# Kernel optimization log

Measured on AMD Instinct MI355X. Metric: run time of the kernel, lower is better.

The kernel has to match this reference:

```python
import jax, jax.numpy as jnp
import numpy as np


def setup_inputs() -> dict:
    key = jax.random.key(0)
    k1, k2 = jax.random.split(key)
    support_features = jax.random.normal(k1, (1000, 5, 512), dtype=jnp.float32)
    query_features = jax.random.normal(k2, (5000, 512), dtype=jnp.float32)
    return {"support_features": support_features, "query_features": query_features, "use_cosine": 1}


def reference(support_features, query_features, use_cosine):
    # Preprocess: mean-center over (classes, shots), then L2-normalize per vector.
    mean = jnp.mean(support_features, axis=(0, 1), keepdims=True)  # [1,1,D]
    s = support_features - mean                                    # [C,S,D]
    q = query_features - mean[0]                                   # [Q,D]
    s = s / jnp.linalg.norm(s, axis=2, keepdims=True)
    q = q / jnp.linalg.norm(q, axis=1, keepdims=True)
    if use_cosine:
        # cosine sims without materializing [C,Q,S,D]; einsum fuses the dot.
        sims = jnp.einsum('csd,qd->cqs', s, q)   # [C,Q,S]
        best = jnp.max(sims, axis=2)             # [C,Q] best shot per class
        return jnp.argmax(best, axis=0)          # [Q] predicted class
    else:
        # euclidean cdist(query[Q,D], support[C,S,D]) -> [C,Q,S]
        d2 = (jnp.sum(q * q, axis=1)[None, :, None]
              + jnp.sum(s * s, axis=2)[:, None, :]
              - 2.0 * jnp.einsum('csd,qd->cqs', s, q))
        dist = jnp.sqrt(jnp.maximum(d2, 0.0))
        best = jnp.min(dist, axis=2)
        return jnp.argmin(best, axis=0)
```

## Files before the change

### kernel.cpp

```cpp
#include <hip/hip_runtime.h>
#include <stdint.h>

#define D     512
#define NSUP  5000
#define NQRY  5000
#define NPAD  5120
#define MEAN_BLOCKS 100
#define ROWS_PER_MEAN_BLOCK 50
#define SCALE 512.0f

#define OFF_SHI     0
#define OFF_SLO     5242880
#define OFF_QHI     10485760
#define OFF_QLO     15728640
#define OFF_PARTIAL 20971520
#define OFF_MEAN    21176320
#define OFF_KEYS    21178368

#define SH_SHI   0
#define SH_SLO   32768
#define SH_QHI   65536
#define SH_QLO   98304
#define SH_KL    131072
#define SH_TOTAL (131072 + 2048)

typedef _Float16 half4v __attribute__((ext_vector_type(4)));
typedef _Float16 half8v __attribute__((ext_vector_type(8)));
typedef float    f32x4  __attribute__((ext_vector_type(4)));

__device__ __forceinline__ unsigned long long pack_key(float v, int sidx) {
    unsigned u = __float_as_uint(v);
    u = (u & 0x80000000u) ? ~u : (u | 0x80000000u);
    return ((unsigned long long)u << 32) | (unsigned)(0xFFFFFFFFu - (unsigned)sidx);
}

__device__ __forceinline__ void gload16(const void* g, void* l) {
    __builtin_amdgcn_global_load_lds(
        (const __attribute__((address_space(1))) unsigned int*)g,
        (__attribute__((address_space(3))) unsigned int*)l, 16, 0, 0);
}

__global__ void k_partial_mean(const float* __restrict__ sup, float* __restrict__ partial) {
    const int col = threadIdx.x;
    const int b   = blockIdx.x;
    const int r0  = b * ROWS_PER_MEAN_BLOCK;
    float acc = 0.0f;
    #pragma unroll 5
    for (int r = 0; r < ROWS_PER_MEAN_BLOCK; ++r)
        acc += sup[(size_t)(r0 + r) * D + col];
    partial[b * D + col] = acc;
}

__global__ void k_mean_init(const float* __restrict__ partial, float* __restrict__ mean,
                            unsigned long long* __restrict__ keys) {
    const int col = threadIdx.x;
    float acc = 0.0f;
    #pragma unroll 4
    for (int b = 0; b < MEAN_BLOCKS; ++b) acc += partial[b * D + col];
    mean[col] = acc * (1.0f / (float)NSUP);
    for (int i = col; i < NSUP; i += 512) keys[i] = 0ull;
}

__global__ void k_split(const float* __restrict__ sup, const float* __restrict__ qry,
                        const float* __restrict__ mean,
                        _Float16* __restrict__ shi, _Float16* __restrict__ slo,
                        _Float16* __restrict__ qhi, _Float16* __restrict__ qlo) {
    const int t    = threadIdx.x;
    const int rloc = t >> 7;
    const int tc   = t & 127;
    const int b    = (int)blockIdx.x * 4 + rloc;
    const float* src; _Float16 *dhi, *dlo; int valid;
    if (b < NPAD) { src = sup + (size_t)b * D;
                    dhi = shi + (size_t)b * D; dlo = slo + (size_t)b * D; valid = (b < NSUP); }
    else          { int r = b - NPAD; src = qry + (size_t)r * D;
                    dhi = qhi + (size_t)r * D; dlo = qlo + (size_t)r * D; valid = (r < NQRY); }
    __shared__ float red[8];
    if (!valid) {
        half4v z = {};
        *(half4v*)(dhi + tc * 4) = z;
        *(half4v*)(dlo + tc * 4) = z;
        return;
    }
    float4 v = *(const float4*)(src + tc * 4);
    float4 m = *(const float4*)(mean + tc * 4);
    v.x -= m.x; v.y -= m.y; v.z -= m.z; v.w -= m.w;
    float ss = v.x * v.x + v.y * v.y + v.z * v.z + v.w * v.w;
    #pragma unroll
    for (int off = 32; off > 0; off >>= 1) ss += __shfl_down(ss, off, 64);
    if ((t & 63) == 0) red[t >> 6] = ss;
    __syncthreads();
    const float rn = SCALE / sqrtf(red[rloc * 2] + red[rloc * 2 + 1]);
    float sv[4] = {v.x * rn, v.y * rn, v.z * rn, v.w * rn};
    half4v h, l;
    #pragma unroll
    for (int i = 0; i < 4; ++i) {
        _Float16 hh = (_Float16)sv[i];
        h[i] = hh;
        l[i] = (_Float16)(sv[i] - (float)hh);
    }
    *(half4v*)(dhi + tc * 4) = h;
    *(half4v*)(dlo + tc * 4) = l;
}

__launch_bounds__(512, 2)
__global__ void k_main(const _Float16* __restrict__ shi, const _Float16* __restrict__ slo,
                       const _Float16* __restrict__ qhi, const _Float16* __restrict__ qlo,
                       unsigned long long* __restrict__ keys) {
    extern __shared__ char smem[];
    char* lshi = smem + SH_SHI;
    char* lslo = smem + SH_SLO;
    char* lqhi = smem + SH_QHI;
    char* lqlo = smem + SH_QLO;
    unsigned long long* kl = (unsigned long long*)(smem + SH_KL);

    const int tid  = threadIdx.x;
    const int lane = tid & 63;
    const int wv   = tid >> 6;
    const int q0   = blockIdx.x * 256;
    const int s0   = blockIdx.y * 256;
    const int wr   = wv >> 2;
    const int wc   = wv & 3;

    if (tid < 256) kl[tid] = 0ull;

    const int srow = wv * 16 + (lane >> 2);
    const int sl0  = ((lane & 3) ^ ((lane >> 3) & 3)) * 16;
    const size_t gA0 = (size_t)(s0 + srow) * 1024 + sl0;
    const size_t gB0 = (size_t)(q0 + srow) * 1024 + sl0;
    const char* pShi = (const char*)shi; const char* pSlo = (const char*)slo;
    const char* pQhi = (const char*)qhi; const char* pQlo = (const char*)qlo;
    const int dst0 = wv * 1024;
    const int dst1 = 8192 + wv * 1024;

    const int l15 = lane & 15;
    const int kg  = lane >> 4;
    const int swz = (kg ^ ((l15 >> 1) & 3)) * 16;
    const int foA = (wr * 128 + l15) * 64 + swz;
    const int foB = (wc * 64  + l15) * 64 + swz;

    f32x4 acc[8][4] = {};

#define BAR()    asm volatile("s_barrier" ::: "memory")
#define WAITV6() asm volatile("s_waitcnt vmcnt(6)" ::: "memory")
#define WAITV4() asm volatile("s_waitcnt vmcnt(4)" ::: "memory")

#define ST2(P, KT, K2) do { const size_t kb_ = (size_t)(KT) * 64;           \
        if ((K2) == 0) {                                                    \
            gload16(pShi + gA0 + kb_,          lshi + (P) * 16384 + dst0);  \
            gload16(pShi + gA0 + 131072 + kb_, lshi + (P) * 16384 + dst1);  \
        } else if ((K2) == 1) {                                             \
            gload16(pSlo + gA0 + kb_,          lslo + (P) * 16384 + dst0);  \
            gload16(pSlo + gA0 + 131072 + kb_, lslo + (P) * 16384 + dst1);  \
        } else if ((K2) == 2) {                                             \
            gload16(pQhi + gB0 + kb_,          lqhi + (P) * 16384 + dst0);  \
            gload16(pQhi + gB0 + 131072 + kb_, lqhi + (P) * 16384 + dst1);  \
        } else {                                                            \
            gload16(pQlo + gB0 + kb_,          lqlo + (P) * 16384 + dst0);  \
            gload16(pQlo + gB0 + 131072 + kb_, lqlo + (P) * 16384 + dst1);  \
        } } while (0)

#define MMA32(AV, BV) do {                                                  \
        __builtin_amdgcn_s_setprio(1);                                      \
        _Pragma("unroll")                                                   \
        for (int fa_ = 0; fa_ < 8; ++fa_)                                   \
        { _Pragma("unroll")                                                 \
          for (int fb_ = 0; fb_ < 4; ++fb_) {                               \
            acc[fa_][fb_] = __builtin_amdgcn_mfma_f32_16x16x32_f16(         \
                AV[fa_], BV[fb_], acc[fa_][fb_], 0, 0, 0);                  \
          } }                                                               \
        __builtin_amdgcn_s_setprio(0);                                      \
        __builtin_amdgcn_sched_barrier(0);                                  \
    } while (0)

    ST2(0, 0, 0); ST2(0, 0, 2); ST2(0, 0, 1); ST2(0, 0, 3);
    WAITV4();
    BAR();

    for (int t = 0; t < 16; ++t) {
        const int P  = t & 1;
        const int Pn = P ^ 1;
        const int tn = (t + 1) & 15;
        half8v ah[8], al[8], bh[4], bl[4];

        #pragma unroll
        for (int f = 0; f < 8; ++f)
            ah[f] = *(const half8v*)(lshi + P * 16384 + foA + f * 1024);
        #pragma unroll
        for (int j = 0; j < 4; ++j)
            bh[j] = *(const half8v*)(lqhi + P * 16384 + foB + j * 1024);
        ST2(Pn, tn, 0);
        ST2(Pn, tn, 2);
        MMA32(ah, bh);
        WAITV6();
        BAR();

        #pragma unroll
        for (int f = 0; f < 8; ++f)
            al[f] = *(const half8v*)(lslo + P * 16384 + foA + f * 1024);
        ST2(Pn, tn, 1);
        MMA32(al, bh);
        WAITV6();
        BAR();

        #pragma unroll
        for (int j = 0; j < 4; ++j)
            bl[j] = *(const half8v*)(lqlo + P * 16384 + foB + j * 1024);
        ST2(Pn, tn, 3);
        MMA32(ah, bl);
        WAITV4();
        BAR();
    }

#undef MMA32
#undef ST2

    #pragma unroll
    for (int fb = 0; fb < 4; ++fb) {
        unsigned long long best = 0ull;
        #pragma unroll
        for (int fa = 0; fa < 8; ++fa)
            #pragma unroll
            for (int r = 0; r < 4; ++r) {
                const int s = s0 + wr * 128 + fa * 16 + kg * 4 + r;
                if (s < NSUP) {
                    unsigned long long k = pack_key(acc[fa][fb][r], s);
                    if (k > best) best = k;
                }
            }
        unsigned long long o = __shfl_xor(best, 16, 64); if (o > best) best = o;
        o = __shfl_xor(best, 32, 64);                    if (o > best) best = o;
        if (kg == 0) atomicMax(&kl[wc * 64 + fb * 16 + l15], best);
    }
    __syncthreads();
    if (tid < 256) {
        const int q = q0 + tid;
        if (q < NQRY && kl[tid] != 0ull) atomicMax(&keys[q], kl[tid]);
    }
#undef BAR
#undef WAITV6
#undef WAITV4
}

__global__ void k_decode(const unsigned long long* __restrict__ keys, int* __restrict__ out) {
    const int q = blockIdx.x * 256 + threadIdx.x;
    if (q < NQRY) {
        unsigned sidx = 0xFFFFFFFFu - (unsigned)(keys[q] & 0xFFFFFFFFull);
        out[q] = (int)(sidx / 5u);
    }
}

extern "C" void kernel_launch(void* const* d_in, const int* in_sizes, int n_in,
                              void* d_out, int out_size, void* d_ws, size_t ws_size,
                              hipStream_t stream) {
    const float* sup = (const float*)d_in[0];
    const float* qry = (const float*)d_in[1];
    int* out = (int*)d_out;

    char* ws = (char*)d_ws;
    _Float16* shi = (_Float16*)(ws + OFF_SHI);
    _Float16* slo = (_Float16*)(ws + OFF_SLO);
    _Float16* qhi = (_Float16*)(ws + OFF_QHI);
    _Float16* qlo = (_Float16*)(ws + OFF_QLO);
    float* partial = (float*)(ws + OFF_PARTIAL);
    float* mean    = (float*)(ws + OFF_MEAN);
    unsigned long long* keys = (unsigned long long*)(ws + OFF_KEYS);

    static bool attr_set = false;
    if (!attr_set) {
        (void)hipFuncSetAttribute((const void*)k_main,
                                  hipFuncAttributeMaxDynamicSharedMemorySize, SH_TOTAL);
        attr_set = true;
    }

    k_partial_mean<<<MEAN_BLOCKS, 512, 0, stream>>>(sup, partial);
    k_mean_init<<<1, 512, 0, stream>>>(partial, mean, keys);
    k_split<<<(2 * NPAD) / 4, 512, 0, stream>>>(sup, qry, mean, shi, slo, qhi, qlo);
    dim3 grid(NPAD / 256, NPAD / 256);
    k_main<<<grid, 512, SH_TOTAL, stream>>>(shi, slo, qhi, qlo, keys);
    k_decode<<<(NQRY + 255) / 256, 256, 0, stream>>>(keys, out);
}
```

Baseline: 163.9 us.

## Fuse mean reduction and decode into neighbours using last-block atomic counters

Merges the partial-mean and mean-finalize kernels into one kernel in which the last block to finish, found through an atomic counter, computes the mean. It also folds the decode step into the tail of the main GEMM kernel with a second last-block counter, and peels the final k-iteration so no wasted prefetch is issued. The aim is to cut two kernel launches and the idle gaps between them, at the cost of an added memset, extra fences, and a serial decode done by a single block.

```diff
diff --git a/kernel.cpp b/kernel.cpp
--- a/kernel.cpp
+++ b/kernel.cpp
@@ -5,8 +5,6 @@
 #define NSUP  5000
 #define NQRY  5000
 #define NPAD  5120
-#define MEAN_BLOCKS 100
-#define ROWS_PER_MEAN_BLOCK 50
 #define SCALE 512.0f
 
 #define OFF_SHI     0
@@ -16,13 +14,15 @@
 #define OFF_PARTIAL 20971520
 #define OFF_MEAN    21176320
 #define OFF_KEYS    21178368
+#define OFF_CTR     21218368
 
 #define SH_SHI   0
 #define SH_SLO   32768
 #define SH_QHI   65536
 #define SH_QLO   98304
 #define SH_KL    131072
-#define SH_TOTAL (131072 + 2048)
+#define SH_DM    133120
+#define SH_TOTAL 133136
 
 typedef _Float16 half4v __attribute__((ext_vector_type(4)));
 typedef _Float16 half8v __attribute__((ext_vector_type(8)));
@@ -40,25 +40,31 @@
         (__attribute__((address_space(3))) unsigned int*)l, 16, 0, 0);
 }
 
-__global__ void k_partial_mean(const float* __restrict__ sup, float* __restrict__ partial) {
+__global__ void k_prep(const float* __restrict__ sup, float* __restrict__ partial,
+                       float* __restrict__ mean, unsigned long long* __restrict__ keys,
+                       unsigned int* __restrict__ ctr) {
     const int col = threadIdx.x;
     const int b   = blockIdx.x;
-    const int r0  = b * ROWS_PER_MEAN_BLOCK;
     float acc = 0.0f;
     #pragma unroll 5
-    for (int r = 0; r < ROWS_PER_MEAN_BLOCK; ++r)
-        acc += sup[(size_t)(r0 + r) * D + col];
+    for (int r = 0; r < 50; ++r)
+        acc += sup[(size_t)(b * 50 + r) * D + col];
     partial[b * D + col] = acc;
-}
-
-__global__ void k_mean_init(const float* __restrict__ partial, float* __restrict__ mean,
-                            unsigned long long* __restrict__ keys) {
-    const int col = threadIdx.x;
-    float acc = 0.0f;
-    #pragma unroll 4
-    for (int b = 0; b < MEAN_BLOCKS; ++b) acc += partial[b * D + col];
-    mean[col] = acc * (1.0f / (float)NSUP);
-    for (int i = col; i < NSUP; i += 512) keys[i] = 0ull;
+    if (col < 50) keys[b * 50 + col] = 0ull;
+    __threadfence();
+    __syncthreads();
+    __shared__ unsigned int done;
+    if (col == 0)
+        done = __hip_atomic_fetch_add(ctr, 1u, __ATOMIC_ACQ_REL, __HIP_MEMORY_SCOPE_AGENT);
+    __syncthreads();
+    if (done == 99) {
+        float m = 0.0f;
+        #pragma unroll 4
+        for (int bb = 0; bb < 100; ++bb)
+            m += __hip_atomic_load(&partial[bb * D + col],
+                                   __ATOMIC_RELAXED, __HIP_MEMORY_SCOPE_AGENT);
+        mean[col] = m * (1.0f / (float)NSUP);
+    }
 }
 
 __global__ void k_split(const float* __restrict__ sup, const float* __restrict__ qry,
@@ -105,7 +111,8 @@
 __launch_bounds__(512, 2)
 __global__ void k_main(const _Float16* __restrict__ shi, const _Float16* __restrict__ slo,
                        const _Float16* __restrict__ qhi, const _Float16* __restrict__ qlo,
-                       unsigned long long* __restrict__ keys) {
+                       unsigned long long* __restrict__ keys, int* __restrict__ out,
+                       unsigned int* __restrict__ ctr) {
     extern __shared__ char smem[];
     char* lshi = smem + SH_SHI;
     char* lslo = smem + SH_SLO;
@@ -143,6 +150,8 @@
 #define BAR()    asm volatile("s_barrier" ::: "memory")
 #define WAITV6() asm volatile("s_waitcnt vmcnt(6)" ::: "memory")
 #define WAITV4() asm volatile("s_waitcnt vmcnt(4)" ::: "memory")
+#define WAITV2() asm volatile("s_waitcnt vmcnt(2)" ::: "memory")
+#define WAITV0() asm volatile("s_waitcnt vmcnt(0)" ::: "memory")
 
 #define ST2(P, KT, K2) do { const size_t kb_ = (size_t)(KT) * 64;           \
         if ((K2) == 0) {                                                    \
@@ -159,6 +168,15 @@
             gload16(pQlo + gB0 + 131072 + kb_, lqlo + (P) * 16384 + dst1);  \
         } } while (0)
 
+#define RD_AH(P) do { _Pragma("unroll") for (int f = 0; f < 8; ++f)         \
+        ah[f] = *(const half8v*)(lshi + (P) * 16384 + foA + f * 1024); } while (0)
+#define RD_AL(P) do { _Pragma("unroll") for (int f = 0; f < 8; ++f)         \
+        al[f] = *(const half8v*)(lslo + (P) * 16384 + foA + f * 1024); } while (0)
+#define RD_BH(P) do { _Pragma("unroll") for (int j = 0; j < 4; ++j)         \
+        bh[j] = *(const half8v*)(lqhi + (P) * 16384 + foB + j * 1024); } while (0)
+#define RD_BL(P) do { _Pragma("unroll") for (int j = 0; j < 4; ++j)         \
+        bl[j] = *(const half8v*)(lqlo + (P) * 16384 + foB + j * 1024); } while (0)
+
 #define MMA32(AV, BV) do {                                                  \
         __builtin_amdgcn_s_setprio(1);                                      \
         _Pragma("unroll")                                                   \
@@ -176,42 +194,47 @@
     WAITV4();
     BAR();
 
-    for (int t = 0; t < 16; ++t) {
+    for (int t = 0; t < 15; ++t) {
         const int P  = t & 1;
         const int Pn = P ^ 1;
-        const int tn = (t + 1) & 15;
+        const int tn = t + 1;
         half8v ah[8], al[8], bh[4], bl[4];
 
-        #pragma unroll
-        for (int f = 0; f < 8; ++f)
-            ah[f] = *(const half8v*)(lshi + P * 16384 + foA + f * 1024);
-        #pragma unroll
-        for (int j = 0; j < 4; ++j)
-            bh[j] = *(const half8v*)(lqhi + P * 16384 + foB + j * 1024);
-        ST2(Pn, tn, 0);
-        ST2(Pn, tn, 2);
+        RD_AH(P); RD_BH(P);
+        ST2(Pn, tn, 0); ST2(Pn, tn, 2);
         MMA32(ah, bh);
         WAITV6();
         BAR();
-
-        #pragma unroll
-        for (int f = 0; f < 8; ++f)
-            al[f] = *(const half8v*)(lslo + P * 16384 + foA + f * 1024);
+        RD_AL(P);
         ST2(Pn, tn, 1);
         MMA32(al, bh);
         WAITV6();
         BAR();
-
-        #pragma unroll
-        for (int j = 0; j < 4; ++j)
-            bl[j] = *(const half8v*)(lqlo + P * 16384 + foB + j * 1024);
+        RD_BL(P);
         ST2(Pn, tn, 3);
         MMA32(ah, bl);
         WAITV4();
         BAR();
     }
+    {
+        half8v ah[8], al[8], bh[4], bl[4];
+        RD_AH(1); RD_BH(1);
+        MMA32(ah, bh);
+        WAITV2();
+        BAR();
+        RD_AL(1);
+        MMA32(al, bh);
+        WAITV0();
+        BAR();
+        RD_BL(1);
+        MMA32(ah, bl);
+    }
 
 #undef MMA32
+#undef RD_BL
+#undef RD_BH
+#undef RD_AL
+#undef RD_AH
 #undef ST2
 
     #pragma unroll
@@ -236,17 +259,26 @@
         const int q = q0 + tid;
         if (q < NQRY && kl[tid] != 0ull) atomicMax(&keys[q], kl[tid]);
     }
+
+    __syncthreads();
+    __threadfence();
+    unsigned int* dmark = (unsigned int*)(smem + SH_DM);
+    if (tid == 0)
+        *dmark = __hip_atomic_fetch_add(ctr, 1u, __ATOMIC_ACQ_REL, __HIP_MEMORY_SCOPE_AGENT);
+    __syncthreads();
+    if (*dmark == (unsigned)(gridDim.x * gridDim.y - 1)) {
+        for (int q = tid; q < NQRY; q += 512) {
+            unsigned long long kv = __hip_atomic_load(&keys[q], __ATOMIC_RELAXED,
+                                                      __HIP_MEMORY_SCOPE_AGENT);
+            unsigned sidx = 0xFFFFFFFFu - (unsigned)(kv & 0xFFFFFFFFull);
+            out[q] = (int)(sidx / 5u);
+        }
+    }
 #undef BAR
 #undef WAITV6
 #undef WAITV4
-}
-
-__global__ void k_decode(const unsigned long long* __restrict__ keys, int* __restrict__ out) {
-    const int q = blockIdx.x * 256 + threadIdx.x;
-    if (q < NQRY) {
-        unsigned sidx = 0xFFFFFFFFu - (unsigned)(keys[q] & 0xFFFFFFFFull);
-        out[q] = (int)(sidx / 5u);
-    }
+#undef WAITV2
+#undef WAITV0
 }
 
 extern "C" void kernel_launch(void* const* d_in, const int* in_sizes, int n_in,
@@ -264,6 +296,7 @@
     float* partial = (float*)(ws + OFF_PARTIAL);
     float* mean    = (float*)(ws + OFF_MEAN);
     unsigned long long* keys = (unsigned long long*)(ws + OFF_KEYS);
+    unsigned int* ctr        = (unsigned int*)(ws + OFF_CTR);
 
     static bool attr_set = false;
     if (!attr_set) {
@@ -272,10 +305,10 @@
         attr_set = true;
     }
 
-    k_partial_mean<<<MEAN_BLOCKS, 512, 0, stream>>>(sup, partial);
-    k_mean_init<<<1, 512, 0, stream>>>(partial, mean, keys);
+    (void)hipMemsetAsync(ctr, 0, 8, stream);
+
+    k_prep<<<100, 512, 0, stream>>>(sup, partial, mean, keys, ctr);
     k_split<<<(2 * NPAD) / 4, 512, 0, stream>>>(sup, qry, mean, shi, slo, qhi, qlo);
     dim3 grid(NPAD / 256, NPAD / 256);
-    k_main<<<grid, 512, SH_TOTAL, stream>>>(shi, slo, qhi, qlo, keys);
-    k_decode<<<(NQRY + 255) / 256, 256, 0, stream>>>(keys, out);
-}
+    k_main<<<grid, 512, SH_TOTAL, stream>>>(shi, slo, qhi, qlo, keys, out, ctr + 1);
+}
```

New measurement: 229.6 us. 40.0% more time.

## Swizzle block-to-tile mapping per XCD and cut pipeline barriers per k-step

Applied to the files above, without the earlier changes.

Launches the main GEMM as a 1D grid of 400 blocks and remaps block ids so that blocks landing on the same XCD (round-robin by id mod 8) work on nearby tiles, with the goal of better L2 reuse. The k-loop stage is reduced from three barriers to two: lo-part loads for both operands are issued together and two MFMA groups run back to back. The wasted wrap-around prefetch on the last iteration is removed by peeling the final tile. This raises register pressure because more fragments are live at once, and the new wait counts need to line up with the outstanding loads.

```diff
diff --git a/kernel.cpp b/kernel.cpp
--- a/kernel.cpp
+++ b/kernel.cpp
@@ -116,8 +116,11 @@
     const int tid  = threadIdx.x;
     const int lane = tid & 63;
     const int wv   = tid >> 6;
-    const int q0   = blockIdx.x * 256;
-    const int s0   = blockIdx.y * 256;
+
+    const int bid = (int)blockIdx.x;
+    const int swz_id = (bid & 7) * 50 + (bid >> 3);
+    const int q0 = (swz_id % 20) * 256;
+    const int s0 = (swz_id / 20) * 256;
     const int wr   = wv >> 2;
     const int wc   = wv & 3;
 
@@ -141,8 +144,8 @@
     f32x4 acc[8][4] = {};
 
 #define BAR()    asm volatile("s_barrier" ::: "memory")
-#define WAITV6() asm volatile("s_waitcnt vmcnt(6)" ::: "memory")
 #define WAITV4() asm volatile("s_waitcnt vmcnt(4)" ::: "memory")
+#define WAITV0() asm volatile("s_waitcnt vmcnt(0)" ::: "memory")
 
 #define ST2(P, KT, K2) do { const size_t kb_ = (size_t)(KT) * 64;           \
         if ((K2) == 0) {                                                    \
@@ -159,6 +162,15 @@
             gload16(pQlo + gB0 + 131072 + kb_, lqlo + (P) * 16384 + dst1);  \
         } } while (0)
 
+#define RD_AH(P) do { _Pragma("unroll") for (int f = 0; f < 8; ++f)         \
+        ah[f] = *(const half8v*)(lshi + (P) * 16384 + foA + f * 1024); } while (0)
+#define RD_AL(P) do { _Pragma("unroll") for (int f = 0; f < 8; ++f)         \
+        al[f] = *(const half8v*)(lslo + (P) * 16384 + foA + f * 1024); } while (0)
+#define RD_BH(P) do { _Pragma("unroll") for (int j = 0; j < 4; ++j)         \
+        bh[j] = *(const half8v*)(lqhi + (P) * 16384 + foB + j * 1024); } while (0)
+#define RD_BL(P) do { _Pragma("unroll") for (int j = 0; j < 4; ++j)         \
+        bl[j] = *(const half8v*)(lqlo + (P) * 16384 + foB + j * 1024); } while (0)
+
 #define MMA32(AV, BV) do {                                                  \
         __builtin_amdgcn_s_setprio(1);                                      \
         _Pragma("unroll")                                                   \
@@ -176,42 +188,40 @@
     WAITV4();
     BAR();
 
-    for (int t = 0; t < 16; ++t) {
+    for (int t = 0; t < 15; ++t) {
         const int P  = t & 1;
         const int Pn = P ^ 1;
-        const int tn = (t + 1) & 15;
+        const int tn = t + 1;
         half8v ah[8], al[8], bh[4], bl[4];
 
-        #pragma unroll
-        for (int f = 0; f < 8; ++f)
-            ah[f] = *(const half8v*)(lshi + P * 16384 + foA + f * 1024);
-        #pragma unroll
-        for (int j = 0; j < 4; ++j)
-            bh[j] = *(const half8v*)(lqhi + P * 16384 + foB + j * 1024);
-        ST2(Pn, tn, 0);
-        ST2(Pn, tn, 2);
+        RD_AH(P); RD_BH(P);
+        ST2(Pn, tn, 0); ST2(Pn, tn, 2);
         MMA32(ah, bh);
-        WAITV6();
+        WAITV4();
         BAR();
-
-        #pragma unroll
-        for (int f = 0; f < 8; ++f)
-            al[f] = *(const half8v*)(lslo + P * 16384 + foA + f * 1024);
-        ST2(Pn, tn, 1);
+        RD_AL(P); RD_BL(P);
+        ST2(Pn, tn, 1); ST2(Pn, tn, 3);
         MMA32(al, bh);
-        WAITV6();
-        BAR();
-
-        #pragma unroll
-        for (int j = 0; j < 4; ++j)
-            bl[j] = *(const half8v*)(lqlo + P * 16384 + foB + j * 1024);
-        ST2(Pn, tn, 3);
         MMA32(ah, bl);
         WAITV4();
         BAR();
     }
+    {
+        half8v ah[8], al[8], bh[4], bl[4];
+        RD_AH(1); RD_BH(1);
+        MMA32(ah, bh);
+        WAITV0();
+        BAR();
+        RD_AL(1); RD_BL(1);
+        MMA32(al, bh);
+        MMA32(ah, bl);
+    }
 
 #undef MMA32
+#undef RD_BL
+#undef RD_BH
+#undef RD_AL
+#undef RD_AH
 #undef ST2
 
     #pragma unroll
@@ -237,8 +247,8 @@
         if (q < NQRY && kl[tid] != 0ull) atomicMax(&keys[q], kl[tid]);
     }
 #undef BAR
-#undef WAITV6
 #undef WAITV4
+#undef WAITV0
 }
 
 __global__ void k_decode(const unsigned long long* __restrict__ keys, int* __restrict__ out) {
@@ -275,7 +285,6 @@
     k_partial_mean<<<MEAN_BLOCKS, 512, 0, stream>>>(sup, partial);
     k_mean_init<<<1, 512, 0, stream>>>(partial, mean, keys);
     k_split<<<(2 * NPAD) / 4, 512, 0, stream>>>(sup, qry, mean, shi, slo, qhi, qlo);
-    dim3 grid(NPAD / 256, NPAD / 256);
-    k_main<<<grid, 512, SH_TOTAL, stream>>>(shi, slo, qhi, qlo, keys);
+    k_main<<<400, 512, SH_TOTAL, stream>>>(shi, slo, qhi, qlo, keys);
     k_decode<<<(NQRY + 255) / 256, 256, 0, stream>>>(keys, out);
 }
```

Result: faster. 158.1 us (-3.5%).
